# Performance work log

Hardware: AMD Instinct MI355X
Metric: run time of the kernel (lower is better)

Reference implementation:

```python
import jax, jax.numpy as jnp
import numpy as np

# ---- dimensions ----
N_MOL, N_PER = 256, 32
N = N_MOL * N_PER                      # 8192 nodes
E = N_MOL * N_PER * (N_PER - 1)        # 253952 fully-connected directed edges
SDIM, VDIM, EDIM = 256, 64, 32
NAF, NBT, LAT = 16, 5, 64
LAYERS = 5
MSG_IN = 2 * SDIM + EDIM + 2           # [s_i, s_j, e, d, a]
MSG_OUT = SDIM + VDIM + 1 + EDIM       # scalar msg, vec weights, pos weight, edge update
BOND_IN = SDIM + EDIM + 1
BOND_HID = 128


def _block_fc_edges():
    # fully-connected (no self loops) edges within each molecule of N_PER atoms
    idx = np.arange(N_PER)
    src, tgt = np.meshgrid(idx, idx, indexing='ij')
    mask = src != tgt
    src, tgt = src[mask], tgt[mask]
    offs = (np.arange(N_MOL) * N_PER)[:, None]
    S = (src[None, :] + offs).reshape(-1)
    T = (tgt[None, :] + offs).reshape(-1)
    return np.stack([S, T], 0).astype(np.int64)


def setup_inputs() -> dict:
    key = jax.random.key(0)
    ks = jax.random.split(key, 16)
    edge_index = jnp.asarray(_block_fc_edges())
    batch = jnp.asarray(np.repeat(np.arange(N_MOL), N_PER).astype(np.int64))
    return dict(
        x=jax.random.normal(ks[0], (N, NAF), jnp.float32),
        z=jax.random.normal(ks[1], (N, LAT), jnp.float32),
        rot=jax.random.normal(ks[2], (N_MOL, 3, 3), jnp.float32),
        edge_index_global=edge_index,
        edge_attr_global=jax.random.normal(ks[3], (E, NBT), jnp.float32),
        batch=batch,
        # atom/bond input mappings (DenseLayer == Linear)
        Wam=jax.random.normal(ks[4], (NAF + LAT, SDIM + 3), jnp.float32) * 0.05,
        bam=jnp.zeros((SDIM + 3,), jnp.float32),
        Wbm=jax.random.normal(ks[5], (NBT, EDIM), jnp.float32) * 0.3,
        bbm=jnp.zeros((EDIM,), jnp.float32),
        # stacked per-layer EQGAT message-MLP weights
        gW1=jax.random.normal(ks[6], (LAYERS, MSG_IN, SDIM), jnp.float32) * 0.03,
        gb1=jnp.zeros((LAYERS, SDIM), jnp.float32),
        gW2=jax.random.normal(ks[7], (LAYERS, SDIM, MSG_OUT), jnp.float32) * 0.05,
        gb2=jnp.zeros((LAYERS, MSG_OUT), jnp.float32),
        # prediction heads
        Wh1=jax.random.normal(ks[8], (SDIM, SDIM), jnp.float32) * 0.05,
        bh1=jnp.zeros((SDIM,), jnp.float32),
        Wh2=jax.random.normal(ks[9], (SDIM, NAF), jnp.float32) * 0.05,
        bh2=jnp.zeros((NAF,), jnp.float32),
        We1=jax.random.normal(ks[10], (BOND_IN, BOND_HID), jnp.float32) * 0.05,
        be1=jnp.zeros((BOND_HID,), jnp.float32),
        We2=jax.random.normal(ks[11], (BOND_HID, NBT), jnp.float32) * 0.05,
        be2=jnp.zeros((NBT,), jnp.float32),
    )


def _edge_attrs(pos, src, tgt):
    # faithful to Decoder.calculate_edge_attrs (sqrt=True)
    r = pos[tgt] - pos[src]                       # [E,3]
    a = jnp.sum(pos[tgt] * pos[src], -1)          # [E]
    d = jnp.sqrt(jnp.clip(jnp.sum(r * r, -1), 1e-6))
    r_norm = r / (1.0 + d)[:, None]
    return d, a, r_norm


def reference(x, z, rot, edge_index_global, edge_attr_global, batch,
              Wam, bam, Wbm, bbm, gW1, gb1, gW2, gb2,
              Wh1, bh1, Wh2, bh2, We1, be1, We2, be2):
    src, tgt = edge_index_global[0], edge_index_global[1]
    n = x.shape[0]
    # atom mapping + split into scalar feats and positions
    h = jnp.concatenate([x, z], -1) @ Wam + bam
    s, pos = h[:, :SDIM], h[:, SDIM:]
    # per-graph rotation of positions
    pos = jnp.einsum('bij,bj->bi', rot[batch], pos)
    # bond mapping
    e = edge_attr_global @ Wbm + bbm
    v = jnp.zeros((n, 3, VDIM), x.dtype)
    # segment-mean denominator (in-degree), fixed since edge_index is fixed
    cnt = jnp.clip(jax.ops.segment_sum(jnp.ones((src.shape[0],), x.dtype), tgt,
                                       num_segments=n), 1.0)

    def seg_mean(m):
        out = jax.ops.segment_sum(m, tgt, num_segments=n)
        return out / cnt.reshape((n,) + (1,) * (m.ndim - 1))

    def layer(carry, p):
        s, v, pos, e = carry
        W1, b1, W2, b2 = p
        d, a, r_norm = _edge_attrs(pos, src, tgt)   # recompute_edge_attributes=True
        feat = jnp.concatenate([s[src], s[tgt], e, d[:, None], a[:, None]], -1)
        hdn = jax.nn.silu(feat @ W1 + b1)
        m = hdn @ W2 + b2
        m_s = m[:, :SDIM]
        m_v = m[:, SDIM:SDIM + VDIM]
        m_p = m[:, SDIM + VDIM:SDIM + VDIM + 1]
        m_e = m[:, SDIM + VDIM + 1:]
        s = s + seg_mean(m_s)                                   # scalar update
        v = v + seg_mean(r_norm[:, :, None] * m_v[:, None, :])  # equivariant vec update
        pos = pos + seg_mean(r_norm * m_p)                      # equivariant pos update
        e = e + m_e                                             # edge feature update
        return (s, v, pos, e), None

    (s, v, pos, e), _ = jax.lax.scan(layer, (s, v, pos, e), (gW1, gb1, gW2, gb2))

    # prediction head: atom logits, bond logits (symmetric s_i+s_j), coords
    atoms = jax.nn.silu(s @ Wh1 + bh1) @ Wh2 + bh2
    d, a, r_norm = _edge_attrs(pos, src, tgt)
    ef = jnp.concatenate([s[src] + s[tgt], e, d[:, None]], -1)
    bonds = jax.nn.silu(ef @ We1 + be1) @ We2 + be2
    return atoms, bonds, pos
```

## Files before the change

kernel.cpp:

```cpp
#include <hip/hip_runtime.h>
#include <hip/hip_bf16.h>
#include <cstdint>
#include <cstddef>

#define N_MOLS 256
#define NN     8192
#define SDIM_  256
#define NAF_   16
#define LAYERS_ 5

typedef __attribute__((ext_vector_type(8)))  short bf16x8;
typedef __attribute__((ext_vector_type(16))) float f32x16;
typedef __attribute__((ext_vector_type(4)))  float f32x4;

__device__ __forceinline__ float silu_f(float x) {
    return x * __builtin_amdgcn_rcpf(1.f + __expf(-x));
}
__device__ __forceinline__ short bfc(float f) {
    __hip_bfloat16 h = __float2bfloat16(f);
    return __builtin_bit_cast(short, h);
}
__device__ __forceinline__ float bf2f(short h) {
    union { uint32_t u; float f; } v; v.u = ((uint32_t)(unsigned short)h) << 16; return v.f;
}
#define ONEBF ((short)0x3F80)

#define OFF_T1    0
#define OFF_W2ST  655360
#define OFF_WH1T  983040
#define OFF_WE1T  1048576
#define OFF_W1CG  1081344
#define OFF_W1DA  1122304
#define OFF_W2P   1124864
#define OFF_W2EI  1126144
#define OFF_WE1CG 1167104
#define OFF_WD    1171200
#define OFF_WE2I  1171328
#define W_TOTAL   1175424

__global__ __launch_bounds__(256) void prep_weights(
    const float* __restrict__ gW1, const float* __restrict__ gW2,
    const float* __restrict__ Wh1, const float* __restrict__ We1,
    const float* __restrict__ We2, short* __restrict__ wb)
{
    for (int o = blockIdx.x * 256 + threadIdx.x; o < W_TOTAL; o += gridDim.x * 256) {
        float v;
        if (o < OFF_W2ST) {
            const int l = o >> 17, r = o & 131071;
            const int j2 = r >> 8, k = r & 255;
            v = gW1[(size_t)l * 139776 + (size_t)((j2 >> 8) * 256 + k) * 256 + (j2 & 255)];
        } else if (o < OFF_WH1T) {
            const int q = o - OFF_W2ST;
            const int l = q >> 16, r = q & 65535;
            const int n = r >> 8, k = r & 255;
            v = gW2[(size_t)l * 90368 + (size_t)k * 353 + n];
        } else if (o < OFF_WE1T) {
            const int q = o - OFF_WH1T;
            v = Wh1[(size_t)(q & 255) * 256 + (q >> 8)];
        } else if (o < OFF_W1CG) {
            const int q = o - OFF_WE1T;
            v = We1[(size_t)(q & 255) * 128 + (q >> 8)];
        } else if (o < OFF_W1DA) {
            const int q = o - OFF_W1CG;
            const int l = q >> 13, r = q & 8191;
            const int j = r >> 5, w = r & 31;
            v = gW1[(size_t)l * 139776 + (size_t)(512 + w) * 256 + j];
        } else if (o < OFF_W2P) {
            const int q = o - OFF_W1DA;
            const int l = q >> 9, r = q & 511;
            v = gW1[(size_t)l * 139776 + (size_t)(544 + (r >> 8)) * 256 + (r & 255)];
        } else if (o < OFF_W2EI) {
            const int q = o - OFF_W2P;
            v = gW2[(size_t)(q >> 8) * 90368 + (size_t)(q & 255) * 353 + 320];
        } else if (o < OFF_WE1CG) {
            const int q = o - OFF_W2EI;
            const int l = q >> 13, r = q & 8191;
            const int kk = r >> 9, lanei = (r >> 3) & 63, jj = r & 7;
            const int j = kk * 16 + (lanei >> 5) * 8 + jj;
            v = gW2[(size_t)l * 90368 + (size_t)j * 353 + 321 + (lanei & 31)];
        } else if (o < OFF_WD) {
            const int q = o - OFF_WE1CG;
            v = We1[(size_t)(256 + (q & 31)) * 128 + (q >> 5)];
        } else if (o < OFF_WE2I) {
            v = We1[288 * 128 + (o - OFF_WD)];
        } else {
            const int q = o - OFF_WE2I;
            const int kk = q >> 9, lanei = (q >> 3) & 63, jj = q & 7;
            const int c = lanei & 31;
            v = (c < 5) ? We2[(size_t)(kk * 16 + (lanei >> 5) * 8 + jj) * 5 + c] : 0.f;
        }
        wb[o] = bfc(v);
    }
}

__global__ __launch_bounds__(256) void node_init2(
    const float* __restrict__ x, const float* __restrict__ z,
    const float* __restrict__ rot, const float* __restrict__ Wam,
    const float* __restrict__ bam, float* __restrict__ s,
    short* __restrict__ sbf, float* __restrict__ pos)
{
    const int mol = blockIdx.x, t = threadIdx.x;
    __shared__ __align__(16) float xz[32][80];
    __shared__ float praw[32][3];
    for (int idx = t; idx < 32 * 80; idx += 256) {
        const int i = idx / 80, k = idx % 80;
        xz[i][k] = (k < 16) ? x[(size_t)(mol * 32 + i) * 16 + k]
                            : z[(size_t)(mol * 32 + i) * 64 + (k - 16)];
    }
    __syncthreads();
    float acc[32];
    #pragma unroll
    for (int i = 0; i < 32; ++i) acc[i] = 0.f;
    for (int k0 = 0; k0 < 80; k0 += 4) {
        const float w0 = Wam[(k0 + 0) * 259 + t];
        const float w1 = Wam[(k0 + 1) * 259 + t];
        const float w2 = Wam[(k0 + 2) * 259 + t];
        const float w3 = Wam[(k0 + 3) * 259 + t];
        #pragma unroll
        for (int i = 0; i < 32; ++i) {
            const float4 xv = *(const float4*)&xz[i][k0];
            acc[i] += xv.x * w0 + xv.y * w1 + xv.z * w2 + xv.w * w3;
        }
    }
    const float bv = bam[t];
    #pragma unroll
    for (int i = 0; i < 32; ++i) {
        const float v = acc[i] + bv;
        s[(size_t)(mol * 32 + i) * 256 + t] = v;
        sbf[(size_t)(mol * 32 + i) * 256 + t] = bfc(v);
    }
    if (t < 96) {
        const int i = t / 3, c = t % 3;
        float a2 = bam[256 + c];
        for (int k = 0; k < 80; ++k) a2 += xz[i][k] * Wam[k * 259 + 256 + c];
        praw[i][c] = a2;
    }
    __syncthreads();
    if (t < 96) {
        const int i = t / 3, c = t % 3;
        float p = 0.f;
        for (int jj = 0; jj < 3; ++jj) p += rot[mol * 9 + c * 3 + jj] * praw[i][jj];
        pos[(size_t)(mol * 32 + i) * 3 + c] = p;
    }
}

__global__ __launch_bounds__(256) void edge_init2(
    const float* __restrict__ ea, const float* __restrict__ Wbm,
    const float* __restrict__ bbm, short* __restrict__ ebuf)
{
    const int tile = blockIdx.x;
    const int mol = tile >> 5, n = tile & 31;
    const int t = threadIdx.x;
    for (int i = t; i < 31 * 32; i += 256) {
        const int rr = i >> 5, c = i & 31;
        const int s_ = rr + (rr >= n ? 1 : 0);
        const int ge = (mol * 32 + s_) * 31 + (n - (n > s_ ? 1 : 0));
        float acc = bbm[c];
        #pragma unroll
        for (int k = 0; k < 5; ++k) acc += ea[(size_t)ge * 5 + k] * Wbm[k * 32 + c];
        ebuf[(size_t)tile * 31 * 32 + i] = bfc(acc);
    }
}

template<int ACT, int OUTBF>
__global__ __launch_bounds__(256) void gemm_mfma(
    const short* __restrict__ A, const short* __restrict__ BT,
    void* __restrict__ Cv, const float* __restrict__ bias,
    int K, int N, float alpha)
{
    const int n0 = blockIdx.x * 64, m0 = blockIdx.y * 128;
    const int t = threadIdx.x;
    const int wave = t >> 6, lane = t & 63;
    const int l = lane & 31, half = lane >> 5;
    const int wm = wave & 1, wn = wave >> 1;
    __shared__ __align__(16) short sA[128][40];
    __shared__ __align__(16) short sBt[64][40];
    f32x16 acc0 = {}, acc1 = {};
    const int mA = t >> 1, koA = (t & 1) * 16;
    const int nB = t & 63, kqB = (t >> 6) * 8;
    for (int k0 = 0; k0 < K; k0 += 32) {
        {
            const short* ap = A + (size_t)(m0 + mA) * K + k0 + koA;
            *(bf16x8*)&sA[mA][koA]     = *(const bf16x8*)(ap);
            *(bf16x8*)&sA[mA][koA + 8] = *(const bf16x8*)(ap + 8);
        }
        {
            const short* bp = BT + (size_t)(n0 + nB) * K + k0 + kqB;
            *(bf16x8*)&sBt[nB][kqB] = *(const bf16x8*)bp;
        }
        __syncthreads();
        #pragma unroll
        for (int ks = 0; ks < 2; ++ks) {
            const bf16x8 bfrag = *(const bf16x8*)&sBt[wn * 32 + l][ks * 16 + half * 8];
            const bf16x8 afr0  = *(const bf16x8*)&sA[wm * 64 + l][ks * 16 + half * 8];
            const bf16x8 afr1  = *(const bf16x8*)&sA[wm * 64 + 32 + l][ks * 16 + half * 8];
            acc0 = __builtin_amdgcn_mfma_f32_32x32x16_bf16(afr0, bfrag, acc0, 0,0,0);
            acc1 = __builtin_amdgcn_mfma_f32_32x32x16_bf16(afr1, bfrag, acc1, 0,0,0);
        }
        __syncthreads();
    }
    const int n = n0 + wn * 32 + l;
    const float bv = bias ? bias[n] : 0.f;
    #pragma unroll
    for (int r = 0; r < 16; ++r) {
        const int row = (r & 3) + 8 * (r >> 2) + 4 * half;
        #pragma unroll
        for (int h = 0; h < 2; ++h) {
            const int m = m0 + wm * 64 + h * 32 + row;
            float v = alpha * (h ? acc1[r] : acc0[r]) + bv;
            if (ACT) v = silu_f(v);
            if (OUTBF) ((short*)Cv)[(size_t)m * N + n] = bfc(v);
            else       ((float*)Cv)[(size_t)m * N + n] = v;
        }
    }
}

__global__ __launch_bounds__(512) void edge_mfma(
    const short* __restrict__ sbfA, const short* __restrict__ T1,
    const float* __restrict__ posIn, float* __restrict__ posOut,
    short* __restrict__ ebuf,
    const short* __restrict__ W1cG, const short* __restrict__ W1daP,
    const short* __restrict__ W2pP, const short* __restrict__ W2eimg,
    const short* __restrict__ W2sT,
    const float* __restrict__ b1, const float* __restrict__ b2,
    float* __restrict__ s, short* __restrict__ sbfOut)
{
    const int blk = blockIdx.x;
    const int mol = blk >> 1;
    const int nbase = (blk & 1) * 16;
    const int t = threadIdx.x;
    const int wave = t >> 6, lane = t & 63;
    const int l = lane & 31, half = lane >> 5;
    const int node0 = mol * 32;

    __shared__ __align__(16) short sBg[256][72];
    __shared__ __align__(16) short sM[8][32][40];
    __shared__ __align__(16) short sHrows[16][264];
    __shared__ __align__(16) short sSB[16][264];
    __shared__ float sPosS[32][4];
    __shared__ __align__(16) short sW1da[2][256];
    __shared__ __align__(16) short sW2p[256];
    __shared__ float sP[8][32];
    __shared__ float sPd[16][4];
    short* sSbf = &sM[0][0][0];

    {
        const int j = t & 255, gh = t >> 8;
        const bf16x8 v0 = *(const bf16x8*)&W1cG[j * 32 + gh * 16];
        const bf16x8 v1 = *(const bf16x8*)&W1cG[j * 32 + gh * 16 + 8];
        const int c3 = (j >> 3) & 3;
        const int s0 = ((gh * 2 + 0) + 3 * c3) & 7;
        const int s1 = ((gh * 2 + 1) + 3 * c3) & 7;
        *(bf16x8*)&sBg[j][s0 * 8] = v0;
        *(bf16x8*)&sBg[j][s1 * 8] = v1;
    }
    {
        const int row = t >> 4, ch = (t & 15) * 16;
        const short* src = sbfA + (size_t)(node0 + row) * 256 + ch;
        *(bf16x8*)&sSbf[row * 264 + ch]     = *(const bf16x8*)(src);
        *(bf16x8*)&sSbf[row * 264 + ch + 8] = *(const bf16x8*)(src + 8);
    }
    if (t < 64) {
        short* d = &sW1da[0][0];
        *(bf16x8*)&d[t * 8] = *(const bf16x8*)&W1daP[t * 8];
    }
    if (t < 32) *(bf16x8*)&sW2p[t * 8] = *(const bf16x8*)&W2pP[t * 8];
    if (t < 96) sPosS[t / 3][t % 3] = posIn[node0 * 3 + t];
    __syncthreads();

    {
        const int jt = wave;
        const int j = jt * 32 + l;
        f32x16 accA = {}, accB = {};
        #pragma unroll
        for (int k0 = 0; k0 < 256; k0 += 16) {
            const bf16x8 afr = *(const bf16x8*)&sSbf[l * 264 + k0 + half * 8];
            const bf16x8 bA  = *(const bf16x8*)(T1 + (size_t)(j) * 256 + k0 + half * 8);
            const bf16x8 bB  = *(const bf16x8*)(T1 + (size_t)(256 + j) * 256 + k0 + half * 8);
            accA = __builtin_amdgcn_mfma_f32_32x32x16_bf16(afr, bA, accA, 0,0,0);
            accB = __builtin_amdgcn_mfma_f32_32x32x16_bf16(afr, bB, accB, 0,0,0);
        }
        const int c3 = (j >> 3) & 3;
        #pragma unroll
        for (int r = 0; r < 16; ++r) {
            const int node = (r & 3) + 8 * (r >> 2) + 4 * half;
            const int k = 32 + node;
            const int slot = ((k >> 3) + 3 * c3) & 7;
            sBg[j][slot * 8 + (k & 7)] = bfc(accA[r]);
            const int nl = node - nbase;
            if ((unsigned)nl < 16u) sSB[nl][j] = bfc(accB[r]);
        }
    }
    __syncthreads();

    bf16x8 w2efr[16];
    #pragma unroll
    for (int kk = 0; kk < 16; ++kk)
        w2efr[kk] = *(const bf16x8*)&W2eimg[(size_t)(kk * 64 + lane) * 8];
    float b1v[8];
    short w1dv[8], w1av[8];
    #pragma unroll
    for (int cb = 0; cb < 8; ++cb) {
        b1v[cb]  = b1[cb * 32 + l];
        w1dv[cb] = sW1da[0][cb * 32 + l];
        w1av[cb] = sW1da[1][cb * 32 + l];
    }
    const float b2e = b2[321 + l];
    const float b2p = b2[320];
    int bslot[4];
    #pragma unroll
    for (int ks = 0; ks < 4; ++ks)
        bslot[ks] = ((ks * 2 + half) + 3 * ((l >> 3) & 3)) & 7;

    for (int ni = 0; ni < 2; ++ni) {
        const int n = nbase + wave + ni * 8;
        const int nloc = wave + ni * 8;
        const int rrc = (l < 31) ? l : 30;
        const int src = rrc + (rrc >= n ? 1 : 0);
        const float ax = sPosS[n][0],  ay = sPosS[n][1],  az = sPosS[n][2];
        const float bx = sPosS[src][0], by = sPosS[src][1], bz = sPosS[src][2];
        const float rx = ax - bx, ry = ay - by, rz = az - bz;
        const float av = ax * bx + ay * by + az * bz;
        const float dd = sqrtf(fmaxf(rx * rx + ry * ry + rz * rz, 1e-6f));
        const float inv = __builtin_amdgcn_rcpf(1.f + dd);
        const float rnx = rx * inv, rny = ry * inv, rnz = rz * inv;

        const short* ebase = ebuf + ((size_t)((mol * 32 + n) * 31 + l)) * 32;
        const bf16x8 fr0 = *(const bf16x8*)(ebase + half * 8);
        const bf16x8 fr1 = *(const bf16x8*)(ebase + 16 + half * 8);
        bf16x8 fr2 = {}, fr3, fr4;
        if (half == 0) { fr2[0] = bfc(dd); fr2[1] = bfc(av); }
        #pragma unroll
        for (int jj = 0; jj < 8; ++jj) {
            fr3[jj] = (half * 8 + jj == src)      ? ONEBF : (short)0;
            fr4[jj] = (16 + half * 8 + jj == src) ? ONEBF : (short)0;
        }

        f32x16 accC = {}, accP = {};
        float Hacc[8];

        const int g = l >> 3, jlow = l & 7;
        #pragma unroll
        for (int cb = 0; cb < 8; ++cb) {
            const float sbv = bf2f(sSB[nloc][cb * 32 + l]) + b1v[cb];
            f32x16 acc;
            #pragma unroll
            for (int r = 0; r < 16; ++r) acc[r] = sbv;
            {
                const short* brow = &sBg[cb * 32 + l][0];
                __builtin_amdgcn_s_setprio(1);
                acc = __builtin_amdgcn_mfma_f32_32x32x16_bf16(fr0, *(const bf16x8*)(brow + bslot[0]*8), acc, 0,0,0);
                acc = __builtin_amdgcn_mfma_f32_32x32x16_bf16(fr1, *(const bf16x8*)(brow + bslot[1]*8), acc, 0,0,0);
                acc = __builtin_amdgcn_mfma_f32_32x32x16_bf16(fr3, *(const bf16x8*)(brow + bslot[2]*8), acc, 0,0,0);
                acc = __builtin_amdgcn_mfma_f32_32x32x16_bf16(fr4, *(const bf16x8*)(brow + bslot[3]*8), acc, 0,0,0);
                bf16x8 frB2 = {};
                if (half == 0) { frB2[0] = w1dv[cb]; frB2[1] = w1av[cb]; }
                acc = __builtin_amdgcn_mfma_f32_32x32x16_bf16(fr2, frB2, acc, 0,0,0);
                __builtin_amdgcn_s_setprio(0);
            }
            float hs = 0.f;
            #pragma unroll
            for (int r = 0; r < 16; ++r) {
                const int e = (r & 3) + 8 * (r >> 2) + 4 * half;
                float h = silu_f(acc[r]);
                if (half == 1 && r == 15) h = 0.f;
                hs += h;
                sM[wave][e][((g + (e >> 3)) & 3) * 8 + jlow] = bfc(h);
            }
            Hacc[cb] = hs;
            #pragma unroll
            for (int q = 0; q < 2; ++q) {
                const bf16x8 afr  = *(const bf16x8*)&sM[wave][l][((q * 2 + half + (l >> 3)) & 3) * 8];
                const bf16x8 wpfr = *(const bf16x8*)&sW2p[cb * 32 + q * 16 + half * 8];
                accC = __builtin_amdgcn_mfma_f32_32x32x16_bf16(afr, w2efr[cb * 2 + q], accC, 0,0,0);
                accP = __builtin_amdgcn_mfma_f32_32x32x16_bf16(afr, wpfr, accP, 0,0,0);
            }
        }
        #pragma unroll
        for (int cb = 0; cb < 8; ++cb) {
            const float v = Hacc[cb] + __shfl_xor(Hacc[cb], 32, 64);
            if (lane < 32) sHrows[nloc][cb * 32 + lane] = bfc(v);
        }
        if (l == 0) {
            #pragma unroll
            for (int q4 = 0; q4 < 4; ++q4) {
                float4 pv = { accP[q4 * 4 + 0], accP[q4 * 4 + 1],
                              accP[q4 * 4 + 2], accP[q4 * 4 + 3] };
                *(float4*)&sP[wave][q4 * 8 + 4 * half] = pv;
            }
        }
        const float pown = sP[wave][l];
        const float pfull = (half == 0 && l < 31) ? (pown + b2p) : 0.f;
        float pd0 = rnx * pfull, pd1 = rny * pfull, pd2 = rnz * pfull;
        #pragma unroll
        for (int m = 1; m <= 32; m <<= 1) {
            pd0 += __shfl_xor(pd0, m, 64);
            pd1 += __shfl_xor(pd1, m, 64);
            pd2 += __shfl_xor(pd2, m, 64);
        }
        if (lane == 0) {
            sPd[nloc][0] = pd0;
            sPd[nloc][1] = pd1;
            sPd[nloc][2] = pd2;
        }
        #pragma unroll
        for (int r = 0; r < 16; ++r) {
            const int e = (r & 3) + 8 * (r >> 2) + 4 * half;
            if (e < 31) {
                short* ep = ebuf + ((size_t)((mol * 32 + n) * 31 + e)) * 32 + l;
                *ep = bfc(bf2f(*ep) + accC[r] + b2e);
            }
        }
    }

    __syncthreads();

    {
        const int jb0 = wave * 32;
        const int arow = lane & 15, kg = lane >> 4;
        f32x4 accS0 = {}, accS1 = {};
        #pragma unroll
        for (int k0 = 0; k0 < 256; k0 += 32) {
            const bf16x8 afr = *(const bf16x8*)&sHrows[arow][k0 + kg * 8];
            const bf16x8 bf0 = *(const bf16x8*)&W2sT[(size_t)(jb0 + arow) * 256 + k0 + kg * 8];
            const bf16x8 bf1 = *(const bf16x8*)&W2sT[(size_t)(jb0 + 16 + arow) * 256 + k0 + kg * 8];
            accS0 = __builtin_amdgcn_mfma_f32_16x16x32_bf16(afr, bf0, accS0, 0,0,0);
            accS1 = __builtin_amdgcn_mfma_f32_16x16x32_bf16(afr, bf1, accS1, 0,0,0);
        }
        const int col = lane & 15;
        const int orow = (lane >> 4) * 4;
        const float bv0 = b2[jb0 + col];
        const float bv1 = b2[jb0 + 16 + col];
        #pragma unroll
        for (int r = 0; r < 4; ++r) {
            const int node = node0 + nbase + orow + r;
            {
                float* sp = s + (size_t)node * 256 + jb0 + col;
                const float nv = *sp + accS0[r] * (1.f / 31.f) + bv0;
                *sp = nv;
                sbfOut[(size_t)node * 256 + jb0 + col] = bfc(nv);
            }
            {
                float* sp = s + (size_t)node * 256 + jb0 + 16 + col;
                const float nv = *sp + accS1[r] * (1.f / 31.f) + bv1;
                *sp = nv;
                sbfOut[(size_t)node * 256 + jb0 + 16 + col] = bfc(nv);
            }
        }
    }
    if (t < 48) {
        const int nl = t / 3, c = t % 3;
        const int node = node0 + nbase + nl;
        posOut[(size_t)node * 3 + c] = posIn[(size_t)node * 3 + c] + sPd[nl][c] * (1.f / 31.f);
    }
}

__global__ __launch_bounds__(512) void bond_mfma(
    const short* __restrict__ U, const float* __restrict__ pos,
    const short* __restrict__ ebuf, const short* __restrict__ We1cG,
    const short* __restrict__ WdP, const short* __restrict__ We2img,
    const float* __restrict__ be1, const float* __restrict__ be2,
    float* __restrict__ outB)
{
    const int blk = blockIdx.x;
    const int mol = blk >> 1;
    const int nbase = (blk & 1) * 16;
    const int t = threadIdx.x;
    const int wave = t >> 6, lane = t & 63;
    const int l = lane & 31, half = lane >> 5;
    const int node0 = mol * 32;

    __shared__ __align__(16) short sBg2[128][72];
    __shared__ __align__(16) short sHdnB[8][32][40];
    __shared__ float sPosS[32][4];
    __shared__ __align__(16) short sWd[128];

    {
        const int j = t & 127, g = t >> 7;
        const bf16x8 v = *(const bf16x8*)&We1cG[j * 32 + g * 8];
        const int slot = (g + 3 * ((j >> 3) & 3)) & 7;
        *(bf16x8*)&sBg2[j][slot * 8] = v;
    }
    {
        const int j = t & 127, kq = t >> 7;
        #pragma unroll
        for (int kk = 0; kk < 8; ++kk) {
            const int k = 32 + kq * 8 + kk;
            const short v = U[(size_t)(node0 + (k - 32)) * 128 + j];
            const int slot = ((k >> 3) + 3 * ((j >> 3) & 3)) & 7;
            sBg2[j][slot * 8 + (k & 7)] = v;
        }
    }
    if (t < 16) *(bf16x8*)&sWd[t * 8] = *(const bf16x8*)&WdP[t * 8];
    if (t < 96) sPosS[t / 3][t % 3] = pos[node0 * 3 + t];

    bf16x8 w2fr[8];
    #pragma unroll
    for (int kk = 0; kk < 8; ++kk)
        w2fr[kk] = *(const bf16x8*)&We2img[(size_t)(kk * 64 + lane) * 8];
    float be1v[4];
    #pragma unroll
    for (int cb = 0; cb < 4; ++cb) be1v[cb] = be1[cb * 32 + l];
    const float be2v = (l < 5) ? be2[l] : 0.f;
    int bslot[4];
    #pragma unroll
    for (int ks = 0; ks < 4; ++ks)
        bslot[ks] = ((ks * 2 + half) + 3 * ((l >> 3) & 3)) & 7;
    __syncthreads();

    for (int ni = 0; ni < 2; ++ni) {
        const int n = nbase + wave + ni * 8;
        const int rrc = (l < 31) ? l : 30;
        const int src = rrc + (rrc >= n ? 1 : 0);
        const float rx = sPosS[n][0] - sPosS[src][0];
        const float ry = sPosS[n][1] - sPosS[src][1];
        const float rz = sPosS[n][2] - sPosS[src][2];
        const float dd = sqrtf(fmaxf(rx * rx + ry * ry + rz * rz, 1e-6f));

        const short* ebase = ebuf + ((size_t)((mol * 32 + n) * 31 + l)) * 32;
        const bf16x8 fr0 = *(const bf16x8*)(ebase + half * 8);
        const bf16x8 fr1 = *(const bf16x8*)(ebase + 16 + half * 8);
        bf16x8 fr2 = {}, fr3, fr4;
        if (half == 0) fr2[0] = bfc(dd);
        #pragma unroll
        for (int jj = 0; jj < 8; ++jj) {
            fr3[jj] = (half * 8 + jj == src)      ? ONEBF : (short)0;
            fr4[jj] = (16 + half * 8 + jj == src) ? ONEBF : (short)0;
        }

        f32x16 accC = {};
        const int g = l >> 3, jlow = l & 7;
        #pragma unroll
        for (int cb = 0; cb < 4; ++cb) {
            const float uin = bf2f(U[(size_t)(node0 + n) * 128 + cb * 32 + l]) + be1v[cb];
            f32x16 acc;
            #pragma unroll
            for (int r = 0; r < 16; ++r) acc[r] = uin;
            {
                const short* brow = &sBg2[cb * 32 + l][0];
                acc = __builtin_amdgcn_mfma_f32_32x32x16_bf16(fr0, *(const bf16x8*)(brow + bslot[0]*8), acc, 0,0,0);
                acc = __builtin_amdgcn_mfma_f32_32x32x16_bf16(fr1, *(const bf16x8*)(brow + bslot[1]*8), acc, 0,0,0);
                acc = __builtin_amdgcn_mfma_f32_32x32x16_bf16(fr3, *(const bf16x8*)(brow + bslot[2]*8), acc, 0,0,0);
                acc = __builtin_amdgcn_mfma_f32_32x32x16_bf16(fr4, *(const bf16x8*)(brow + bslot[3]*8), acc, 0,0,0);
                bf16x8 frWd = {};
                if (half == 0) frWd[0] = sWd[cb * 32 + l];
                acc = __builtin_amdgcn_mfma_f32_32x32x16_bf16(fr2, frWd, acc, 0,0,0);
            }
            #pragma unroll
            for (int r = 0; r < 16; ++r) {
                const int e = (r & 3) + 8 * (r >> 2) + 4 * half;
                sHdnB[wave][e][((g + (e >> 3)) & 3) * 8 + jlow] = bfc(silu_f(acc[r]));
            }
            #pragma unroll
            for (int q = 0; q < 2; ++q) {
                const bf16x8 afr = *(const bf16x8*)&sHdnB[wave][l][((q * 2 + half + (l >> 3)) & 3) * 8];
                accC = __builtin_amdgcn_mfma_f32_32x32x16_bf16(afr, w2fr[cb * 2 + q], accC, 0,0,0);
            }
        }
        if (l < 5) {
            #pragma unroll
            for (int r = 0; r < 16; ++r) {
                const int e = (r & 3) + 8 * (r >> 2) + 4 * half;
                if (e < 31) {
                    const int s_ = e + (e >= n ? 1 : 0);
                    const int ge = (mol * 32 + s_) * 31 + (n - (n > s_ ? 1 : 0));
                    outB[(size_t)ge * 5 + l] = accC[r] + be2v;
                }
            }
        }
    }
}

__global__ __launch_bounds__(256) void pos_copy(const float* __restrict__ pos,
                                                float* __restrict__ out)
{
    const int i = blockIdx.x * 256 + threadIdx.x;
    out[i] = pos[i];
}

__global__ __launch_bounds__(256) void atoms_kernel(
    const short* __restrict__ tmp, const float* __restrict__ Wh2,
    const float* __restrict__ bh2, float* __restrict__ outA)
{
    const int t = threadIdx.x;
    __shared__ __align__(16) float sW[256][17];
    for (int i = t; i < 256 * 4; i += 256) {
        const int k = i >> 2, c4 = (i & 3) * 4;
        const float4 w = *(const float4*)&Wh2[k * 16 + c4];
        sW[k][c4 + 0] = w.x; sW[k][c4 + 1] = w.y;
        sW[k][c4 + 2] = w.z; sW[k][c4 + 3] = w.w;
    }
    __syncthreads();
    const int gid = blockIdx.x * 256 + t;
    const int n = gid >> 4, o = gid & 15;
    float acc = bh2[o];
    for (int k0 = 0; k0 < 256; k0 += 8) {
        const bf16x8 a = *(const bf16x8*)&tmp[(size_t)n * 256 + k0];
        #pragma unroll
        for (int j = 0; j < 8; ++j)
            acc += bf2f(a[j]) * sW[k0 + j][o];
    }
    outA[gid] = acc;
}

extern "C" void kernel_launch(void* const* d_in, const int* in_sizes, int n_in,
                              void* d_out, int out_size, void* d_ws, size_t ws_size,
                              hipStream_t stream) {
    const float* x   = (const float*)d_in[0];
    const float* z   = (const float*)d_in[1];
    const float* rot = (const float*)d_in[2];
    const float* ea  = (const float*)d_in[4];
    const float* Wam = (const float*)d_in[6];
    const float* bam = (const float*)d_in[7];
    const float* Wbm = (const float*)d_in[8];
    const float* bbm = (const float*)d_in[9];
    const float* gW1 = (const float*)d_in[10];
    const float* gb1 = (const float*)d_in[11];
    const float* gW2 = (const float*)d_in[12];
    const float* gb2 = (const float*)d_in[13];
    const float* Wh1 = (const float*)d_in[14];
    const float* bh1 = (const float*)d_in[15];
    const float* Wh2 = (const float*)d_in[16];
    const float* bh2 = (const float*)d_in[17];
    const float* We1 = (const float*)d_in[18];
    const float* be1 = (const float*)d_in[19];
    const float* We2 = (const float*)d_in[20];
    const float* be2 = (const float*)d_in[21];
    float* out = (float*)d_out;

    float* ws  = (float*)d_ws;
    float* s    = ws;
    float* pos  = ws + 2097152;
    short* e    = (short*)(ws + 2121728);
    short* wb   = (short*)(ws + 6184960);
    short* sbf0 = (short*)(ws + 6772672);
    short* sbf1 = (short*)(ws + 10248192);
    short* tmph = (short*)(ws + 12345344);
    short* Uh   = (short*)(ws + 14442496);
    float* pos2 = ws + 16539648;

    prep_weights<<<1024, 256, 0, stream>>>(gW1, gW2, Wh1, We1, We2, wb);
    node_init2<<<N_MOLS, 256, 0, stream>>>(x, z, rot, Wam, bam, s, sbf0, pos);
    edge_init2<<<NN, 256, 0, stream>>>(ea, Wbm, bbm, e);

    float* pbuf[2] = { pos, pos2 };
    short* sbb[2] = { sbf0, sbf1 };
    for (int l = 0; l < LAYERS_; ++l) {
        const float* b1 = gb1 + l * 256;
        const float* b2 = gb2 + l * 353;
        edge_mfma<<<2 * N_MOLS, 512, 0, stream>>>(
            sbb[l & 1], wb + OFF_T1 + (size_t)l * 131072,
            pbuf[l & 1], pbuf[(l + 1) & 1], e,
            wb + OFF_W1CG + l * 8192, wb + OFF_W1DA + l * 512,
            wb + OFF_W2P + l * 256, wb + OFF_W2EI + l * 8192,
            wb + OFF_W2ST + (size_t)l * 65536,
            b1, b2, s, sbb[(l + 1) & 1]);
    }
    float* posF = pbuf[LAYERS_ & 1];
    short* sbfF = sbb[LAYERS_ & 1];

    gemm_mfma<1,1><<<dim3(4, 64), 256, 0, stream>>>(
        sbfF, wb + OFF_WH1T, tmph, bh1, 256, 256, 1.f);
    atoms_kernel<<<512, 256, 0, stream>>>(tmph, Wh2, bh2, out);

    gemm_mfma<0,1><<<dim3(2, 64), 256, 0, stream>>>(
        sbfF, wb + OFF_WE1T, Uh, nullptr, 256, 128, 1.f);
    bond_mfma<<<2 * N_MOLS, 512, 0, stream>>>(
        Uh, posF, e, wb + OFF_WE1CG, wb + OFF_WD, wb + OFF_WE2I,
        be1, be2, out + 131072);

    pos_copy<<<96, 256, 0, stream>>>(posF, out + 131072 + 1269760);
}
```

Baseline: 673.2 us.

## Fuse bond U-GEMM and pos copy into bond kernel; per-molecule edge init

```diff
diff --git a/kernel.cpp b/kernel.cpp
--- a/kernel.cpp
+++ b/kernel.cpp
@@ -144,21 +144,29 @@
     }
 }
 
-__global__ __launch_bounds__(256) void edge_init2(
+__global__ __launch_bounds__(256) void edge_init3(
     const float* __restrict__ ea, const float* __restrict__ Wbm,
     const float* __restrict__ bbm, short* __restrict__ ebuf)
 {
-    const int tile = blockIdx.x;
-    const int mol = tile >> 5, n = tile & 31;
-    const int t = threadIdx.x;
-    for (int i = t; i < 31 * 32; i += 256) {
-        const int rr = i >> 5, c = i & 31;
+    const int mol = blockIdx.x, t = threadIdx.x;
+    __shared__ float sEa[4960];
+    __shared__ float sW[5][32];
+    __shared__ float sB[32];
+    const float* base = ea + (size_t)mol * 4960;
+    for (int i = t; i < 4960; i += 256) sEa[i] = base[i];
+    if (t < 160) sW[t / 32][t & 31] = Wbm[t];
+    if (t < 32)  sB[t] = bbm[t];
+    __syncthreads();
+    for (int i = t; i < 31744; i += 256) {
+        const int c = i & 31;
+        const int rrn = i >> 5;
+        const int n = rrn / 31, rr = rrn - n * 31;
         const int s_ = rr + (rr >= n ? 1 : 0);
-        const int ge = (mol * 32 + s_) * 31 + (n - (n > s_ ? 1 : 0));
-        float acc = bbm[c];
-        #pragma unroll
-        for (int k = 0; k < 5; ++k) acc += ea[(size_t)ge * 5 + k] * Wbm[k * 32 + c];
-        ebuf[(size_t)tile * 31 * 32 + i] = bfc(acc);
+        const int gl = s_ * 31 + (n - (n > s_ ? 1 : 0));
+        float acc = sB[c];
+        #pragma unroll
+        for (int k = 0; k < 5; ++k) acc += sEa[gl * 5 + k] * sW[k][c];
+        ebuf[(size_t)mol * 31744 + i] = bfc(acc);
     }
 }
 
@@ -456,11 +464,12 @@
 }
 
 __global__ __launch_bounds__(512) void bond_mfma(
-    const short* __restrict__ U, const float* __restrict__ pos,
-    const short* __restrict__ ebuf, const short* __restrict__ We1cG,
-    const short* __restrict__ WdP, const short* __restrict__ We2img,
+    const short* __restrict__ sbfA, const short* __restrict__ We1T,
+    const float* __restrict__ pos, short* __restrict__ ebuf,
+    const short* __restrict__ We1cG, const short* __restrict__ WdP,
+    const short* __restrict__ We2img,
     const float* __restrict__ be1, const float* __restrict__ be2,
-    float* __restrict__ outB)
+    float* __restrict__ outB, float* __restrict__ outPos)
 {
     const int blk = blockIdx.x;
     const int mol = blk >> 1;
@@ -472,8 +481,10 @@
 
     __shared__ __align__(16) short sBg2[128][72];
     __shared__ __align__(16) short sHdnB[8][32][40];
+    __shared__ __align__(16) short sU[32][136];
     __shared__ float sPosS[32][4];
     __shared__ __align__(16) short sWd[128];
+    short* sSbf = &sHdnB[0][0][0];
 
     {
         const int j = t & 127, g = t >> 7;
@@ -482,17 +493,35 @@
         *(bf16x8*)&sBg2[j][slot * 8] = v;
     }
     {
-        const int j = t & 127, kq = t >> 7;
-        #pragma unroll
-        for (int kk = 0; kk < 8; ++kk) {
-            const int k = 32 + kq * 8 + kk;
-            const short v = U[(size_t)(node0 + (k - 32)) * 128 + j];
-            const int slot = ((k >> 3) + 3 * ((j >> 3) & 3)) & 7;
-            sBg2[j][slot * 8 + (k & 7)] = v;
-        }
+        const int row = t >> 4, ch = (t & 15) * 16;
+        const short* src = sbfA + (size_t)(node0 + row) * 256 + ch;
+        *(bf16x8*)&sSbf[row * 264 + ch]     = *(const bf16x8*)(src);
+        *(bf16x8*)&sSbf[row * 264 + ch + 8] = *(const bf16x8*)(src + 8);
     }
     if (t < 16) *(bf16x8*)&sWd[t * 8] = *(const bf16x8*)&WdP[t * 8];
     if (t < 96) sPosS[t / 3][t % 3] = pos[node0 * 3 + t];
+    __syncthreads();
+
+    if (wave < 4) {
+        const int j = wave * 32 + l;
+        f32x16 accU = {};
+        #pragma unroll
+        for (int k0 = 0; k0 < 256; k0 += 16) {
+            const bf16x8 afr = *(const bf16x8*)&sSbf[l * 264 + k0 + half * 8];
+            const bf16x8 bU  = *(const bf16x8*)(We1T + (size_t)j * 256 + k0 + half * 8);
+            accU = __builtin_amdgcn_mfma_f32_32x32x16_bf16(afr, bU, accU, 0,0,0);
+        }
+        const int c3 = (j >> 3) & 3;
+        #pragma unroll
+        for (int r = 0; r < 16; ++r) {
+            const int node = (r & 3) + 8 * (r >> 2) + 4 * half;
+            const short uv = bfc(accU[r]);
+            const int k = 32 + node;
+            const int slot = ((k >> 3) + 3 * c3) & 7;
+            sBg2[j][slot * 8 + (k & 7)] = uv;
+            sU[node][j] = uv;
+        }
+    }
 
     bf16x8 w2fr[8];
     #pragma unroll
@@ -532,7 +561,7 @@
         const int g = l >> 3, jlow = l & 7;
         #pragma unroll
         for (int cb = 0; cb < 4; ++cb) {
-            const float uin = bf2f(U[(size_t)(node0 + n) * 128 + cb * 32 + l]) + be1v[cb];
+            const float uin = bf2f(sU[n][cb * 32 + l]) + be1v[cb];
             f32x16 acc;
             #pragma unroll
             for (int r = 0; r < 16; ++r) acc[r] = uin;
@@ -569,13 +598,11 @@
             }
         }
     }
-}
-
-__global__ __launch_bounds__(256) void pos_copy(const float* __restrict__ pos,
-                                                float* __restrict__ out)
-{
-    const int i = blockIdx.x * 256 + threadIdx.x;
-    out[i] = pos[i];
+    if (t < 48) {
+        const int nl = t / 3, c = t % 3;
+        const int node = node0 + nbase + nl;
+        outPos[(size_t)node * 3 + c] = pos[(size_t)node * 3 + c];
+    }
 }
 
 __global__ __launch_bounds__(256) void atoms_kernel(
@@ -636,12 +663,11 @@
     short* sbf0 = (short*)(ws + 6772672);
     short* sbf1 = (short*)(ws + 10248192);
     short* tmph = (short*)(ws + 12345344);
-    short* Uh   = (short*)(ws + 14442496);
     float* pos2 = ws + 16539648;
 
     prep_weights<<<1024, 256, 0, stream>>>(gW1, gW2, Wh1, We1, We2, wb);
     node_init2<<<N_MOLS, 256, 0, stream>>>(x, z, rot, Wam, bam, s, sbf0, pos);
-    edge_init2<<<NN, 256, 0, stream>>>(ea, Wbm, bbm, e);
+    edge_init3<<<N_MOLS, 256, 0, stream>>>(ea, Wbm, bbm, e);
 
     float* pbuf[2] = { pos, pos2 };
     short* sbb[2] = { sbf0, sbf1 };
@@ -663,11 +689,7 @@
         sbfF, wb + OFF_WH1T, tmph, bh1, 256, 256, 1.f);
     atoms_kernel<<<512, 256, 0, stream>>>(tmph, Wh2, bh2, out);
 
-    gemm_mfma<0,1><<<dim3(2, 64), 256, 0, stream>>>(
-        sbfF, wb + OFF_WE1T, Uh, nullptr, 256, 128, 1.f);
     bond_mfma<<<2 * N_MOLS, 512, 0, stream>>>(
-        Uh, posF, e, wb + OFF_WE1CG, wb + OFF_WD, wb + OFF_WE2I,
-        be1, be2, out + 131072);
-
-    pos_copy<<<96, 256, 0, stream>>>(posF, out + 131072 + 1269760);
-}
+        sbfF, wb + OFF_WE1T, posF, e, wb + OFF_WE1CG, wb + OFF_WD,
+        wb + OFF_WE2I, be1, be2, out + 131072, out + 131072 + 1269760);
+}
```

Result: no change. 669.0 us (-0.6%).
